# Performance work log

Measured on AMD Instinct MI355X. Metric: run time of the kernel, lower is better.

Reference implementation:

```python
import jax, jax.numpy as jnp
import numpy as np

DIM = 192; H = 6; HD = DIM // H; WS = 8; N = WS * WS; B = 2048; NW = 64
SCALE = HD ** -0.5


def _rel_idx():
    # replicates torch meshgrid (indexing='ij') relative position index
    coords = np.stack(np.meshgrid(np.arange(WS), np.arange(WS), indexing='ij'))  # [2,WS,WS]
    flat = coords.reshape(2, -1)  # [2, N]
    rel = flat[:, :, None] - flat[:, None, :]  # [2, N, N]
    rel = rel.transpose(1, 2, 0).astype(np.int64)
    rel[..., 0] += WS - 1
    rel[..., 1] += WS - 1
    rel[..., 0] *= 2 * WS - 1
    return jnp.asarray(rel.sum(-1), dtype=jnp.int32)  # [N, N]


def setup_inputs() -> dict:
    key = jax.random.key(0)
    ks = jax.random.split(key, 8)
    x1 = jax.random.normal(ks[0], (B, N, DIM), jnp.float32)
    x2 = jax.random.normal(ks[1], (B, N, DIM), jnp.float32)
    mask = jnp.zeros((NW, N, N), jnp.float32)
    qw = jax.random.normal(ks[2], (DIM, DIM), jnp.float32) * 0.02
    qb = jnp.zeros((DIM,), jnp.float32)
    kvw = jax.random.normal(ks[3], (2 * DIM, DIM), jnp.float32) * 0.02
    kvb = jnp.zeros((2 * DIM,), jnp.float32)
    rpb = jax.random.normal(ks[4], ((2 * WS - 1) * (2 * WS - 1), H), jnp.float32) * 0.02
    gamma = jnp.full((1,), 0.5, jnp.float32)  # nonzero to exercise LAM path
    pw = jax.random.normal(ks[5], (DIM, DIM), jnp.float32) * 0.02
    pb = jnp.zeros((DIM,), jnp.float32)
    rel_idx = _rel_idx()
    return {"x1": x1, "x2": x2, "mask": mask, "qw": qw, "qb": qb, "kvw": kvw,
            "kvb": kvb, "rpb": rpb, "gamma": gamma, "pw": pw, "pb": pb,
            "rel_idx": rel_idx}


def reference(x1, x2, mask, qw, qb, kvw, kvb, rpb, gamma, pw, pb, rel_idx):
    # q projection -> [B, H, N, HD], pre-scaled (torch code reassigns q = q*scale)
    q = (x1 @ qw.T + qb).reshape(B, N, H, HD).transpose(0, 2, 1, 3) * SCALE
    kv = (x2 @ kvw.T + kvb).reshape(B, N, 2, H, HD)
    k = kv[:, :, 0].transpose(0, 2, 1, 3)  # [B, H, N, HD]
    v = kv[:, :, 1].transpose(0, 2, 1, 3)
    attn = jnp.einsum('bhnd,bhmd->bhnm', q, k)  # [B, H, N, N]
    # gathered relative position bias [H, N, N]
    bias = rpb[rel_idx.reshape(-1)].reshape(N, N, H).transpose(2, 0, 1)
    attn = attn + bias[None]
    attn = attn.reshape(B // NW, NW, H, N, N) + mask[None, :, None]
    attn = jax.nn.softmax(attn.reshape(B, H, N, N), axis=-1)
    y = jnp.einsum('bhnm,bhmd->bhnd', attn, v)  # [B, H, N, HD]
    # LAM module: channel-wise (dim) attention over (head*num)
    xp = y.transpose(0, 3, 1, 2)              # [B, HD, H, N]
    flat = xp.reshape(B, HD, H * N)
    energy = jnp.einsum('bik,bjk->bij', flat, flat)  # [B, HD, HD]
    # note: original computes energy_new but softmaxes raw energy; replicate
    att = jax.nn.softmax(energy, axis=-1)
    out = jnp.einsum('bij,bjk->bik', att, flat).reshape(B, HD, H, N)
    out = gamma * out + xp
    lam = out.transpose(0, 2, 3, 1)            # [B, H, N, HD]
    x = (lam.transpose(0, 2, 1, 3).reshape(B, N, DIM)
         + q.transpose(0, 2, 1, 3).reshape(B, N, DIM)
         + x1)
    return x @ pw.T + pb
```

## Files before the change

kernel.cpp:

```cpp
#include <hip/hip_runtime.h>

#define DIM 192
#define NTOK 64
#define NHEAD 6
#define HDIM 32
#define SCALE 0.17677669529663687f

typedef __attribute__((ext_vector_type(8))) short bf16x8;
typedef __attribute__((ext_vector_type(4))) float f32x4;

__device__ __forceinline__ ushort f2bf(float f) {
    union { float f; unsigned u; } x; x.f = f;
    unsigned r = x.u + 0x7FFFu + ((x.u >> 16) & 1u);
    return (ushort)(r >> 16);
}
__device__ __forceinline__ float bf2f(ushort h) {
    union { unsigned u; float f; } x; x.u = ((unsigned)h) << 16;
    return x.f;
}

__device__ __forceinline__ f32x4 MF(bf16x8 a, bf16x8 b, f32x4 c) {
    return __builtin_amdgcn_mfma_f32_16x16x32_bf16(a, b, c, 0, 0, 0);
}

__device__ __forceinline__ bf16x8 frag(const ushort* base, int stride, int r0, int k0) {
    const int l = threadIdx.x & 63;
    return *(const bf16x8*)(base + (r0 + (l & 15)) * stride + (k0 + ((l >> 4) << 3)));
}

__global__ void prep_weights(const float* __restrict__ qw, const float* __restrict__ kvw,
                             const float* __restrict__ pw, ushort* __restrict__ wbf) {
    int i = blockIdx.x * 256 + threadIdx.x;
    if (i < 36864) wbf[i] = f2bf(qw[i]);
    else if (i < 110592) wbf[i] = f2bf(kvw[i - 36864]);
    else if (i < 147456) wbf[i] = f2bf(pw[i - 110592]);
}

__global__ void prep_cmb(const float* __restrict__ rpb, const float* __restrict__ mask,
                         ushort* __restrict__ cmb) {
    int t = blockIdx.x * 256 + threadIdx.x;
    int e = t << 2;
    int n0 = e & 63;
    int m  = (e >> 6) & 63;
    int hw = e >> 12;
    int h = hw % 6, w = hw / 6;
#pragma unroll
    for (int j = 0; j < 4; ++j) {
        int n = n0 + j;
        int ridx = ((n >> 3) - (m >> 3) + 7) * 15 + ((n & 7) - (m & 7) + 7);
        float v = rpb[ridx * 6 + h] + mask[(w * 64 + n) * 64 + m];
        cmb[e + j] = f2bf(v);
    }
}

__global__ __launch_bounds__(256, 4) void proj7(
    const float* __restrict__ x1, const float* __restrict__ x2,
    const float* __restrict__ qb, const float* __restrict__ kvb,
    const ushort* __restrict__ qwbf, const ushort* __restrict__ kvwbf,
    ushort* __restrict__ Qf, ushort* __restrict__ Kf, ushort* __restrict__ Vf)
{
    __shared__ __align__(16) ushort sXA[64 * 200];
    __shared__ __align__(16) ushort stg[4 * 1280];
    const int tid = threadIdx.x, wave = tid >> 6, lane = tid & 63;
    const int g = lane >> 4, mcol = lane & 15;
    const int b = blockIdx.x;
    const f32x4 zero4 = {0.f, 0.f, 0.f, 0.f};
    ushort* st = stg + wave * 1280;

    {
        const float4* src = (const float4*)(x2 + (size_t)b * 12288);
        for (int i = tid; i < 3072; i += 256) {
            float4 v = src[i];
            int e = i << 2; int n = e / DIM; int c = e - n * DIM;
            ushort4 w;
            ((ushort*)&w)[0] = f2bf(v.x); ((ushort*)&w)[1] = f2bf(v.y);
            ((ushort*)&w)[2] = f2bf(v.z); ((ushort*)&w)[3] = f2bf(v.w);
            *(ushort4*)(&sXA[n * 200 + c]) = w;
        }
    }
    __syncthreads();

    for (int t = wave; t < 12; t += 4) {
        const int isV = (t >= 6) ? 1 : 0;
        const int h = isV ? (t - 6) : t;
        bf16x8 wf[2][6];
#pragma unroll
        for (int c2 = 0; c2 < 2; ++c2) {
            int ctg = (isV ? (12 + 2 * h) : (2 * h)) + c2;
#pragma unroll
            for (int ks = 0; ks < 6; ++ks)
                wf[c2][ks] = frag(kvwbf, DIM, ctg * 16, ks * 32);
        }
        f32x4 acc[4][2];
#pragma unroll
        for (int rt = 0; rt < 4; ++rt)
#pragma unroll
            for (int c2 = 0; c2 < 2; ++c2) acc[rt][c2] = zero4;
#pragma unroll
        for (int rt = 0; rt < 4; ++rt) {
            bf16x8 af[6];
#pragma unroll
            for (int ks = 0; ks < 6; ++ks) af[ks] = frag(sXA, 200, rt * 16, ks * 32);
#pragma unroll
            for (int c2 = 0; c2 < 2; ++c2)
#pragma unroll
                for (int ks = 0; ks < 6; ++ks)
                    acc[rt][c2] = MF(af[ks], wf[c2][ks], acc[rt][c2]);
        }
        if (!isV) {
#pragma unroll
            for (int ph = 0; ph < 2; ++ph) {
#pragma unroll
                for (int c2 = 0; c2 < 2; ++c2) {
                    float bv = kvb[h * 32 + c2 * 16 + mcol];
#pragma unroll
                    for (int rl = 0; rl < 2; ++rl)
#pragma unroll
                        for (int j = 0; j < 4; ++j)
                            st[(rl * 16 + (g << 2) + j) * 40 + c2 * 16 + mcol] =
                                f2bf(acc[2 * ph + rl][c2][j] + bv);
                }
                asm volatile("s_waitcnt lgkmcnt(0)" ::: "memory");
#pragma unroll
                for (int cl = 0; cl < 2; ++cl) {
                    bf16x8 fr = frag(st, 40, cl * 16, 0);
                    *(bf16x8*)(Kf + ((size_t)(b * 6 + h) * 4 + 2 * ph + cl) * 512 + lane * 8) = fr;
                }
            }
        } else {
#pragma unroll
            for (int c = 0; c < 2; ++c) {
#pragma unroll
                for (int c2 = 0; c2 < 2; ++c2) {
                    float bv = kvb[192 + h * 32 + c2 * 16 + mcol];
#pragma unroll
                    for (int rl = 0; rl < 2; ++rl) {
                        ushort4 w4;
#pragma unroll
                        for (int j = 0; j < 4; ++j)
                            ((ushort*)&w4)[j] = f2bf(acc[2 * c + rl][c2][j] + bv);
                        *(ushort4*)(&st[(c2 * 16 + mcol) * 40 + rl * 16 + (g << 2)]) = w4;
                    }
                }
                asm volatile("s_waitcnt lgkmcnt(0)" ::: "memory");
#pragma unroll
                for (int ctd = 0; ctd < 2; ++ctd) {
                    bf16x8 fr = frag(st, 40, ctd * 16, 0);
                    *(bf16x8*)(Vf + (((size_t)(b * 6 + h) * 2 + c) * 2 + ctd) * 512 + lane * 8) = fr;
                }
            }
        }
    }
    __syncthreads();

    {
        const float4* src = (const float4*)(x1 + (size_t)b * 12288);
        for (int i = tid; i < 3072; i += 256) {
            float4 v = src[i];
            int e = i << 2; int n = e / DIM; int c = e - n * DIM;
            ushort4 w;
            ((ushort*)&w)[0] = f2bf(v.x); ((ushort*)&w)[1] = f2bf(v.y);
            ((ushort*)&w)[2] = f2bf(v.z); ((ushort*)&w)[3] = f2bf(v.w);
            *(ushort4*)(&sXA[n * 200 + c]) = w;
        }
    }
    __syncthreads();

    for (int t = wave; t < 6; t += 4) {
        const int h = t;
        bf16x8 wf[2][6];
#pragma unroll
        for (int c2 = 0; c2 < 2; ++c2)
#pragma unroll
            for (int ks = 0; ks < 6; ++ks)
                wf[c2][ks] = frag(qwbf, DIM, (2 * h + c2) * 16, ks * 32);
        f32x4 acc[4][2];
#pragma unroll
        for (int rt = 0; rt < 4; ++rt)
#pragma unroll
            for (int c2 = 0; c2 < 2; ++c2) acc[rt][c2] = zero4;
#pragma unroll
        for (int rt = 0; rt < 4; ++rt) {
            bf16x8 af[6];
#pragma unroll
            for (int ks = 0; ks < 6; ++ks) af[ks] = frag(sXA, 200, rt * 16, ks * 32);
#pragma unroll
            for (int c2 = 0; c2 < 2; ++c2)
#pragma unroll
                for (int ks = 0; ks < 6; ++ks)
                    acc[rt][c2] = MF(af[ks], wf[c2][ks], acc[rt][c2]);
        }
#pragma unroll
        for (int ph = 0; ph < 2; ++ph) {
#pragma unroll
            for (int c2 = 0; c2 < 2; ++c2) {
                float bv = qb[h * 32 + c2 * 16 + mcol];
#pragma unroll
                for (int rl = 0; rl < 2; ++rl)
#pragma unroll
                    for (int j = 0; j < 4; ++j)
                        st[(rl * 16 + (g << 2) + j) * 40 + c2 * 16 + mcol] =
                            f2bf((acc[2 * ph + rl][c2][j] + bv) * SCALE);
            }
            asm volatile("s_waitcnt lgkmcnt(0)" ::: "memory");
#pragma unroll
            for (int cl = 0; cl < 2; ++cl) {
                bf16x8 fr = frag(st, 40, cl * 16, 0);
                *(bf16x8*)(Qf + ((size_t)(b * 6 + h) * 4 + 2 * ph + cl) * 512 + lane * 8) = fr;
            }
        }
    }
}

__global__ __launch_bounds__(256, 4) void attn_heads(
    const ushort* __restrict__ Qf, ushort* KfY,
    const ushort* __restrict__ Vf, const ushort* __restrict__ cmb)
{
    __shared__ __align__(16) ushort sP[4 * 1280];
    const int tid = threadIdx.x, wave = tid >> 6, lane = tid & 63;
    const int g = lane >> 4, mcol = lane & 15;
    const int gid = blockIdx.x * 4 + wave;
    const int w = gid / 6, h = gid - 6 * (gid / 6);
    const f32x4 zero4 = {0.f, 0.f, 0.f, 0.f};

    const ushort* qp = Qf  + (size_t)gid * 2048;
    ushort*       kp = KfY + (size_t)gid * 2048;
    const ushort* vp = Vf  + (size_t)gid * 2048;
    const ushort* cp = cmb + (size_t)((w & 63) * 6 + h) * 4096;
    ushort* slot = sP + wave * 1280;

    bf16x8 kb[4], vb[4];
#pragma unroll
    for (int ct = 0; ct < 4; ++ct) kb[ct] = *(const bf16x8*)(kp + ct * 512 + lane * 8);
#pragma unroll
    for (int c = 0; c < 4; ++c) vb[c] = *(const bf16x8*)(vp + c * 512 + lane * 8);

    ushort4 y4[4][2];
#pragma unroll
    for (int rt = 0; rt < 4; ++rt) {
        bf16x8 qa = *(const bf16x8*)(qp + rt * 512 + lane * 8);
        f32x4 acc[4];
#pragma unroll
        for (int ct = 0; ct < 4; ++ct) acc[ct] = MF(qa, kb[ct], zero4);
#pragma unroll
        for (int ct = 0; ct < 4; ++ct) {
            ushort4 b4 = *(const ushort4*)(cp + (ct * 16 + mcol) * 64 + rt * 16 + (g << 2));
#pragma unroll
            for (int j = 0; j < 4; ++j) acc[ct][j] += bf2f(((ushort*)&b4)[j]);
        }
        float sm[4];
#pragma unroll
        for (int j = 0; j < 4; ++j) {
            float v = fmaxf(fmaxf(acc[0][j], acc[1][j]), fmaxf(acc[2][j], acc[3][j]));
            v = fmaxf(v, __shfl_xor(v, 1, 64));
            v = fmaxf(v, __shfl_xor(v, 2, 64));
            v = fmaxf(v, __shfl_xor(v, 4, 64));
            v = fmaxf(v, __shfl_xor(v, 8, 64));
            float s = 0.f;
#pragma unroll
            for (int ct = 0; ct < 4; ++ct) {
                float p = __expf(acc[ct][j] - v);
                acc[ct][j] = p; s += p;
            }
            s += __shfl_xor(s, 1, 64);
            s += __shfl_xor(s, 2, 64);
            s += __shfl_xor(s, 4, 64);
            s += __shfl_xor(s, 8, 64);
            sm[j] = 1.0f / s;
        }
#pragma unroll
        for (int ct = 0; ct < 4; ++ct)
#pragma unroll
            for (int j = 0; j < 4; ++j)
                slot[((g << 2) + j) * 72 + ct * 16 + mcol] = f2bf(acc[ct][j] * sm[j]);
        asm volatile("s_waitcnt lgkmcnt(0)" ::: "memory");
        f32x4 ay0 = zero4, ay1 = zero4;
#pragma unroll
        for (int c = 0; c < 2; ++c) {
            bf16x8 pa = frag(slot, 72, 0, c * 32);
            ay0 = MF(pa, vb[c * 2 + 0], ay0);
            ay1 = MF(pa, vb[c * 2 + 1], ay1);
        }
#pragma unroll
        for (int j = 0; j < 4; ++j) {
            ((ushort*)&y4[rt][0])[j] = f2bf(ay0[j]);
            ((ushort*)&y4[rt][1])[j] = f2bf(ay1[j]);
        }
    }
#pragma unroll
    for (int rt = 0; rt < 4; ++rt)
#pragma unroll
        for (int ctd = 0; ctd < 2; ++ctd)
            *(ushort4*)(kp + (ctd * 16 + mcol) * 64 + rt * 16 + (g << 2)) = y4[rt][ctd];
}

__global__ __launch_bounds__(256, 4) void lam_proj(
    const ushort* __restrict__ Yd, const ushort* __restrict__ Qf,
    const float* __restrict__ x1, const float* __restrict__ gammap,
    const ushort* __restrict__ pwbf, const float* __restrict__ pb,
    float* __restrict__ out)
{
    __shared__ __align__(16) ushort sYF[13824];
    __shared__ __align__(16) float  sE[32 * 33];
    __shared__ __align__(16) ushort sAtt[32 * 40];

    const int tid = threadIdx.x, wave = tid >> 6, lane = tid & 63;
    const int g = lane >> 4, mcol = lane & 15;
    const int b = blockIdx.x;
    const float gamma = gammap[0];
    const f32x4 zero4 = {0.f, 0.f, 0.f, 0.f};

    {
        const ushort* src = Yd + (size_t)b * 12288;
        for (int i = tid; i < 1536; i += 256) {
            int hd = i >> 8;
            int rem = i & 255;
            int row = rem >> 3, k8 = rem & 7;
            uint4 v = *(const uint4*)(src + hd * 2048 + row * 64 + k8 * 8);
            *(uint4*)(&sYF[hd * 2304 + row * 72 + k8 * 8]) = v;
        }
    }
    __syncthreads();

    {
        int rt = wave >> 1, ct = wave & 1;
        f32x4 a0 = zero4, a1 = zero4;
#pragma unroll
        for (int hd = 0; hd < 6; hd += 2) {
            const ushort* Y0 = sYF + hd * 2304;
            const ushort* Y1 = sYF + (hd + 1) * 2304;
#pragma unroll
            for (int kk = 0; kk < 2; ++kk) {
                a0 = MF(frag(Y0, 72, rt * 16, kk * 32), frag(Y0, 72, ct * 16, kk * 32), a0);
                a1 = MF(frag(Y1, 72, rt * 16, kk * 32), frag(Y1, 72, ct * 16, kk * 32), a1);
            }
        }
        f32x4 acc = a0 + a1;
#pragma unroll
        for (int j = 0; j < 4; ++j)
            sE[(rt * 16 + (g << 2) + j) * 33 + ct * 16 + mcol] = acc[j];
    }
    __syncthreads();

    {
        int r = tid >> 3, l8 = tid & 7;
        float e[4];
        float mx = -1e30f;
#pragma unroll
        for (int k = 0; k < 4; ++k) { e[k] = sE[r * 33 + l8 + k * 8]; mx = fmaxf(mx, e[k]); }
        mx = fmaxf(mx, __shfl_xor(mx, 1, 64));
        mx = fmaxf(mx, __shfl_xor(mx, 2, 64));
        mx = fmaxf(mx, __shfl_xor(mx, 4, 64));
        float s = 0.f;
#pragma unroll
        for (int k = 0; k < 4; ++k) { e[k] = __expf(e[k] - mx); s += e[k]; }
        s += __shfl_xor(s, 1, 64);
        s += __shfl_xor(s, 2, 64);
        s += __shfl_xor(s, 4, 64);
        float rs = 1.0f / s;
#pragma unroll
        for (int k = 0; k < 4; ++k) sAtt[r * 40 + l8 + k * 8] = f2bf(e[k] * rs);
    }
    __syncthreads();

    bf16x8 aa01[2];
    aa01[0] = frag(sAtt, 40, 0, 0);
    aa01[1] = frag(sAtt, 40, 16, 0);
    ushort4 w4st[12];
#pragma unroll
    for (int i = 0; i < 12; ++i) {
        int t = wave + i * 4;
        int rtL = t & 1, ct = t >> 1;
        int col = ct * 16 + mcol;
        int hh = col >> 6, nn = col & 63;
        const ushort* Yh = sYF + hh * 2304;
        bf16x8 bb;
#pragma unroll
        for (int jj = 0; jj < 8; ++jj) bb[jj] = (short)Yh[((g << 3) + jj) * 72 + nn];
        f32x4 acc = MF(aa01[rtL], bb, zero4);
        int d0 = rtL * 16 + (g << 2);
        ushort4 qv4 = *(const ushort4*)(Qf + (size_t)(b * 6 + hh) * 2048 +
                                        (nn >> 4) * 512 + ((nn & 15) + ((d0 >> 3) << 4)) * 8 + (d0 & 7));
        float4 xv4 = *(const float4*)(x1 + (size_t)b * 12288 + nn * 192 + hh * 32 + d0);
        ushort4 w4;
#pragma unroll
        for (int j = 0; j < 4; ++j) {
            float flatv = bf2f(Yh[(d0 + j) * 72 + nn]);
            float val = gamma * acc[j] + flatv + bf2f(((ushort*)&qv4)[j]) + ((const float*)&xv4)[j];
            ((ushort*)&w4)[j] = f2bf(val);
        }
        w4st[i] = w4;
    }
    __syncthreads();
#pragma unroll
    for (int i = 0; i < 12; ++i) {
        int t = wave + i * 4;
        int rtL = t & 1, ct = t >> 1;
        int col = ct * 16 + mcol;
        int hh = col >> 6, nn = col & 63;
        int d0 = rtL * 16 + (g << 2);
        *(ushort4*)(&sYF[nn * 200 + hh * 32 + d0]) = w4st[i];
    }
    __syncthreads();

    {
        float* outp = out + (size_t)b * 12288;
        const int rt = wave;
        bf16x8 af[6];
#pragma unroll
        for (int ks = 0; ks < 6; ++ks) af[ks] = frag(sYF, 200, rt * 16, ks * 32);
#pragma unroll 2
        for (int ct = 0; ct < 12; ++ct) {
            f32x4 acc = zero4;
#pragma unroll
            for (int ks = 0; ks < 6; ++ks)
                acc = MF(af[ks], frag(pwbf, DIM, ct * 16, ks * 32), acc);
            int co = ct * 16 + mcol;
            float pbv = pb[co];
#pragma unroll
            for (int j = 0; j < 4; ++j)
                outp[(rt * 16 + (g << 2) + j) * DIM + co] = acc[j] + pbv;
        }
    }
}

extern "C" void kernel_launch(void* const* d_in, const int* in_sizes, int n_in,
                              void* d_out, int out_size, void* d_ws, size_t ws_size,
                              hipStream_t stream) {
    const float* x1    = (const float*)d_in[0];
    const float* x2    = (const float*)d_in[1];
    const float* mask  = (const float*)d_in[2];
    const float* qw    = (const float*)d_in[3];
    const float* qbv   = (const float*)d_in[4];
    const float* kvw   = (const float*)d_in[5];
    const float* kvbv  = (const float*)d_in[6];
    const float* rpb   = (const float*)d_in[7];
    const float* gamma = (const float*)d_in[8];
    const float* pw    = (const float*)d_in[9];
    const float* pbv   = (const float*)d_in[10];
    ushort* wbf = (ushort*)d_ws;

    prep_weights<<<576, 256, 0, stream>>>(qw, kvw, pw, wbf);

    ushort* cmb = wbf + 147456;
    ushort* Qf  = wbf + 1720320;
    ushort* Kf  = wbf + 26886144;
    ushort* Vf  = wbf + 52051968;
    prep_cmb<<<1536, 256, 0, stream>>>(rpb, mask, cmb);
    proj7<<<2048, 256, 0, stream>>>(x1, x2, qbv, kvbv,
                                    wbf, wbf + 36864, Qf, Kf, Vf);
    attn_heads<<<3072, 256, 0, stream>>>(Qf, Kf, Vf, cmb);
    lam_proj<<<2048, 256, 0, stream>>>(Kf, Qf, x1, gamma,
                                       wbf + 110592, pbv, (float*)d_out);
}
```

Before: 269.7 us.

## Split projection into separate Q and KV blocks and precompute Q+x1 residual

The projection kernel now launches two blocks per batch element, one handling the K/V projection from x2 and one handling the Q projection from x1, instead of doing both sequentially in one block. This gives more parallelism and a shorter critical path per block. When the workspace is large enough, the Q block also writes a bf16 residual buffer holding q plus the bf16-rounded x1, so lam_proj reads one bf16 value instead of Q plus fp32 x1. The cost is an extra global write of the residual buffer and a larger grid, with slight extra rounding because x1 is added in bf16.

```diff
diff --git a/kernel.cpp b/kernel.cpp
--- a/kernel.cpp
+++ b/kernel.cpp
@@ -53,22 +53,24 @@
     }
 }
 
-__global__ __launch_bounds__(256, 4) void proj7(
+__global__ __launch_bounds__(256, 4) void proj7s(
     const float* __restrict__ x1, const float* __restrict__ x2,
     const float* __restrict__ qb, const float* __restrict__ kvb,
     const ushort* __restrict__ qwbf, const ushort* __restrict__ kvwbf,
-    ushort* __restrict__ Qf, ushort* __restrict__ Kf, ushort* __restrict__ Vf)
+    ushort* __restrict__ Qf, ushort* __restrict__ Kf, ushort* __restrict__ Vf,
+    ushort* __restrict__ Rf, int hasRf)
 {
     __shared__ __align__(16) ushort sXA[64 * 200];
     __shared__ __align__(16) ushort stg[4 * 1280];
     const int tid = threadIdx.x, wave = tid >> 6, lane = tid & 63;
     const int g = lane >> 4, mcol = lane & 15;
-    const int b = blockIdx.x;
+    const int b = blockIdx.x >> 1;
+    const int isQ = blockIdx.x & 1;
     const f32x4 zero4 = {0.f, 0.f, 0.f, 0.f};
     ushort* st = stg + wave * 1280;
 
     {
-        const float4* src = (const float4*)(x2 + (size_t)b * 12288);
+        const float4* src = (const float4*)((isQ ? x1 : x2) + (size_t)b * 12288);
         for (int i = tid; i < 3072; i += 256) {
             float4 v = src[i];
             int e = i << 2; int n = e / DIM; int c = e - n * DIM;
@@ -80,133 +82,143 @@
     }
     __syncthreads();
 
-    for (int t = wave; t < 12; t += 4) {
-        const int isV = (t >= 6) ? 1 : 0;
-        const int h = isV ? (t - 6) : t;
-        bf16x8 wf[2][6];
-#pragma unroll
-        for (int c2 = 0; c2 < 2; ++c2) {
-            int ctg = (isV ? (12 + 2 * h) : (2 * h)) + c2;
-#pragma unroll
-            for (int ks = 0; ks < 6; ++ks)
-                wf[c2][ks] = frag(kvwbf, DIM, ctg * 16, ks * 32);
-        }
-        f32x4 acc[4][2];
-#pragma unroll
-        for (int rt = 0; rt < 4; ++rt)
-#pragma unroll
-            for (int c2 = 0; c2 < 2; ++c2) acc[rt][c2] = zero4;
-#pragma unroll
-        for (int rt = 0; rt < 4; ++rt) {
-            bf16x8 af[6];
-#pragma unroll
-            for (int ks = 0; ks < 6; ++ks) af[ks] = frag(sXA, 200, rt * 16, ks * 32);
+    if (!isQ) {
+        for (int t = wave; t < 12; t += 4) {
+            const int isV = (t >= 6) ? 1 : 0;
+            const int h = isV ? (t - 6) : t;
+            bf16x8 wf[2][6];
+#pragma unroll
+            for (int c2 = 0; c2 < 2; ++c2) {
+                int ctg = (isV ? (12 + 2 * h) : (2 * h)) + c2;
+#pragma unroll
+                for (int ks = 0; ks < 6; ++ks)
+                    wf[c2][ks] = frag(kvwbf, DIM, ctg * 16, ks * 32);
+            }
+            f32x4 acc[4][2];
+#pragma unroll
+            for (int rt = 0; rt < 4; ++rt)
+#pragma unroll
+                for (int c2 = 0; c2 < 2; ++c2) acc[rt][c2] = zero4;
+#pragma unroll
+            for (int rt = 0; rt < 4; ++rt) {
+                bf16x8 af[6];
+#pragma unroll
+                for (int ks = 0; ks < 6; ++ks) af[ks] = frag(sXA, 200, rt * 16, ks * 32);
+#pragma unroll
+                for (int c2 = 0; c2 < 2; ++c2)
+#pragma unroll
+                    for (int ks = 0; ks < 6; ++ks)
+                        acc[rt][c2] = MF(af[ks], wf[c2][ks], acc[rt][c2]);
+            }
+            if (!isV) {
+#pragma unroll
+                for (int ph = 0; ph < 2; ++ph) {
+#pragma unroll
+                    for (int c2 = 0; c2 < 2; ++c2) {
+                        float bv = kvb[h * 32 + c2 * 16 + mcol];
+#pragma unroll
+                        for (int rl = 0; rl < 2; ++rl)
+#pragma unroll
+                            for (int j = 0; j < 4; ++j)
+                                st[(rl * 16 + (g << 2) + j) * 40 + c2 * 16 + mcol] =
+                                    f2bf(acc[2 * ph + rl][c2][j] + bv);
+                    }
+                    asm volatile("s_waitcnt lgkmcnt(0)" ::: "memory");
+#pragma unroll
+                    for (int cl = 0; cl < 2; ++cl) {
+                        bf16x8 fr = frag(st, 40, cl * 16, 0);
+                        *(bf16x8*)(Kf + ((size_t)(b * 6 + h) * 4 + 2 * ph + cl) * 512 + lane * 8) = fr;
+                    }
+                }
+            } else {
+#pragma unroll
+                for (int c = 0; c < 2; ++c) {
+#pragma unroll
+                    for (int c2 = 0; c2 < 2; ++c2) {
+                        float bv = kvb[192 + h * 32 + c2 * 16 + mcol];
+#pragma unroll
+                        for (int rl = 0; rl < 2; ++rl) {
+                            ushort4 w4;
+#pragma unroll
+                            for (int j = 0; j < 4; ++j)
+                                ((ushort*)&w4)[j] = f2bf(acc[2 * c + rl][c2][j] + bv);
+                            *(ushort4*)(&st[(c2 * 16 + mcol) * 40 + rl * 16 + (g << 2)]) = w4;
+                        }
+                    }
+                    asm volatile("s_waitcnt lgkmcnt(0)" ::: "memory");
+#pragma unroll
+                    for (int ctd = 0; ctd < 2; ++ctd) {
+                        bf16x8 fr = frag(st, 40, ctd * 16, 0);
+                        *(bf16x8*)(Vf + (((size_t)(b * 6 + h) * 2 + c) * 2 + ctd) * 512 + lane * 8) = fr;
+                    }
+                }
+            }
+        }
+    } else {
+        for (int t = wave; t < 6; t += 4) {
+            const int h = t;
+            bf16x8 wf[2][6];
 #pragma unroll
             for (int c2 = 0; c2 < 2; ++c2)
 #pragma unroll
                 for (int ks = 0; ks < 6; ++ks)
-                    acc[rt][c2] = MF(af[ks], wf[c2][ks], acc[rt][c2]);
-        }
-        if (!isV) {
+                    wf[c2][ks] = frag(qwbf, DIM, (2 * h + c2) * 16, ks * 32);
+            f32x4 acc[4][2];
+#pragma unroll
+            for (int rt = 0; rt < 4; ++rt)
+#pragma unroll
+                for (int c2 = 0; c2 < 2; ++c2) acc[rt][c2] = zero4;
+#pragma unroll
+            for (int rt = 0; rt < 4; ++rt) {
+                bf16x8 af[6];
+#pragma unroll
+                for (int ks = 0; ks < 6; ++ks) af[ks] = frag(sXA, 200, rt * 16, ks * 32);
+#pragma unroll
+                for (int c2 = 0; c2 < 2; ++c2)
+#pragma unroll
+                    for (int ks = 0; ks < 6; ++ks)
+                        acc[rt][c2] = MF(af[ks], wf[c2][ks], acc[rt][c2]);
+            }
 #pragma unroll
             for (int ph = 0; ph < 2; ++ph) {
 #pragma unroll
                 for (int c2 = 0; c2 < 2; ++c2) {
-                    float bv = kvb[h * 32 + c2 * 16 + mcol];
+                    float bv = qb[h * 32 + c2 * 16 + mcol];
 #pragma unroll
                     for (int rl = 0; rl < 2; ++rl)
 #pragma unroll
                         for (int j = 0; j < 4; ++j)
                             st[(rl * 16 + (g << 2) + j) * 40 + c2 * 16 + mcol] =
-                                f2bf(acc[2 * ph + rl][c2][j] + bv);
+                                f2bf((acc[2 * ph + rl][c2][j] + bv) * SCALE);
                 }
                 asm volatile("s_waitcnt lgkmcnt(0)" ::: "memory");
 #pragma unroll
                 for (int cl = 0; cl < 2; ++cl) {
                     bf16x8 fr = frag(st, 40, cl * 16, 0);
-                    *(bf16x8*)(Kf + ((size_t)(b * 6 + h) * 4 + 2 * ph + cl) * 512 + lane * 8) = fr;
+                    *(bf16x8*)(Qf + ((size_t)(b * 6 + h) * 4 + 2 * ph + cl) * 512 + lane * 8) = fr;
                 }
-            }
-        } else {
-#pragma unroll
-            for (int c = 0; c < 2; ++c) {
-#pragma unroll
-                for (int c2 = 0; c2 < 2; ++c2) {
-                    float bv = kvb[192 + h * 32 + c2 * 16 + mcol];
-#pragma unroll
-                    for (int rl = 0; rl < 2; ++rl) {
-                        ushort4 w4;
-#pragma unroll
-                        for (int j = 0; j < 4; ++j)
-                            ((ushort*)&w4)[j] = f2bf(acc[2 * c + rl][c2][j] + bv);
-                        *(ushort4*)(&st[(c2 * 16 + mcol) * 40 + rl * 16 + (g << 2)]) = w4;
+                if (hasRf) {
+#pragma unroll
+                    for (int c2 = 0; c2 < 2; ++c2) {
+                        float bv = qb[h * 32 + c2 * 16 + mcol];
+#pragma unroll
+                        for (int rl = 0; rl < 2; ++rl)
+#pragma unroll
+                            for (int j = 0; j < 4; ++j) {
+                                int row = 2 * ph + rl;
+                                float qv = (acc[row][c2][j] + bv) * SCALE;
+                                float xv = bf2f(sXA[(ph * 32 + rl * 16 + (g << 2) + j) * 200 +
+                                                    h * 32 + c2 * 16 + mcol]);
+                                st[(rl * 16 + (g << 2) + j) * 40 + c2 * 16 + mcol] = f2bf(qv + xv);
+                            }
+                    }
+                    asm volatile("s_waitcnt lgkmcnt(0)" ::: "memory");
+#pragma unroll
+                    for (int cl = 0; cl < 2; ++cl) {
+                        bf16x8 fr = frag(st, 40, cl * 16, 0);
+                        *(bf16x8*)(Rf + ((size_t)(b * 6 + h) * 4 + 2 * ph + cl) * 512 + lane * 8) = fr;
                     }
                 }
-                asm volatile("s_waitcnt lgkmcnt(0)" ::: "memory");
-#pragma unroll
-                for (int ctd = 0; ctd < 2; ++ctd) {
-                    bf16x8 fr = frag(st, 40, ctd * 16, 0);
-                    *(bf16x8*)(Vf + (((size_t)(b * 6 + h) * 2 + c) * 2 + ctd) * 512 + lane * 8) = fr;
-                }
-            }
-        }
-    }
-    __syncthreads();
-
-    {
-        const float4* src = (const float4*)(x1 + (size_t)b * 12288);
-        for (int i = tid; i < 3072; i += 256) {
-            float4 v = src[i];
-            int e = i << 2; int n = e / DIM; int c = e - n * DIM;
-            ushort4 w;
-            ((ushort*)&w)[0] = f2bf(v.x); ((ushort*)&w)[1] = f2bf(v.y);
-            ((ushort*)&w)[2] = f2bf(v.z); ((ushort*)&w)[3] = f2bf(v.w);
-            *(ushort4*)(&sXA[n * 200 + c]) = w;
-        }
-    }
-    __syncthreads();
-
-    for (int t = wave; t < 6; t += 4) {
-        const int h = t;
-        bf16x8 wf[2][6];
-#pragma unroll
-        for (int c2 = 0; c2 < 2; ++c2)
-#pragma unroll
-            for (int ks = 0; ks < 6; ++ks)
-                wf[c2][ks] = frag(qwbf, DIM, (2 * h + c2) * 16, ks * 32);
-        f32x4 acc[4][2];
-#pragma unroll
-        for (int rt = 0; rt < 4; ++rt)
-#pragma unroll
-            for (int c2 = 0; c2 < 2; ++c2) acc[rt][c2] = zero4;
-#pragma unroll
-        for (int rt = 0; rt < 4; ++rt) {
-            bf16x8 af[6];
-#pragma unroll
-            for (int ks = 0; ks < 6; ++ks) af[ks] = frag(sXA, 200, rt * 16, ks * 32);
-#pragma unroll
-            for (int c2 = 0; c2 < 2; ++c2)
-#pragma unroll
-                for (int ks = 0; ks < 6; ++ks)
-                    acc[rt][c2] = MF(af[ks], wf[c2][ks], acc[rt][c2]);
-        }
-#pragma unroll
-        for (int ph = 0; ph < 2; ++ph) {
-#pragma unroll
-            for (int c2 = 0; c2 < 2; ++c2) {
-                float bv = qb[h * 32 + c2 * 16 + mcol];
-#pragma unroll
-                for (int rl = 0; rl < 2; ++rl)
-#pragma unroll
-                    for (int j = 0; j < 4; ++j)
-                        st[(rl * 16 + (g << 2) + j) * 40 + c2 * 16 + mcol] =
-                            f2bf((acc[2 * ph + rl][c2][j] + bv) * SCALE);
-            }
-            asm volatile("s_waitcnt lgkmcnt(0)" ::: "memory");
-#pragma unroll
-            for (int cl = 0; cl < 2; ++cl) {
-                bf16x8 fr = frag(st, 40, cl * 16, 0);
-                *(bf16x8*)(Qf + ((size_t)(b * 6 + h) * 4 + 2 * ph + cl) * 512 + lane * 8) = fr;
             }
         }
     }
@@ -298,7 +310,7 @@
     const ushort* __restrict__ Yd, const ushort* __restrict__ Qf,
     const float* __restrict__ x1, const float* __restrict__ gammap,
     const ushort* __restrict__ pwbf, const float* __restrict__ pb,
-    float* __restrict__ out)
+    float* __restrict__ out, const ushort* __restrict__ Rf, int useRf)
 {
     __shared__ __align__(16) ushort sYF[13824];
     __shared__ __align__(16) float  sE[32 * 33];
@@ -379,15 +391,26 @@
         for (int jj = 0; jj < 8; ++jj) bb[jj] = (short)Yh[((g << 3) + jj) * 72 + nn];
         f32x4 acc = MF(aa01[rtL], bb, zero4);
         int d0 = rtL * 16 + (g << 2);
-        ushort4 qv4 = *(const ushort4*)(Qf + (size_t)(b * 6 + hh) * 2048 +
-                                        (nn >> 4) * 512 + ((nn & 15) + ((d0 >> 3) << 4)) * 8 + (d0 & 7));
-        float4 xv4 = *(const float4*)(x1 + (size_t)b * 12288 + nn * 192 + hh * 32 + d0);
         ushort4 w4;
-#pragma unroll
-        for (int j = 0; j < 4; ++j) {
-            float flatv = bf2f(Yh[(d0 + j) * 72 + nn]);
-            float val = gamma * acc[j] + flatv + bf2f(((ushort*)&qv4)[j]) + ((const float*)&xv4)[j];
-            ((ushort*)&w4)[j] = f2bf(val);
+        if (useRf) {
+            ushort4 rv4 = *(const ushort4*)(Rf + (size_t)(b * 6 + hh) * 2048 +
+                                            (nn >> 4) * 512 + ((nn & 15) + ((d0 >> 3) << 4)) * 8 + (d0 & 7));
+#pragma unroll
+            for (int j = 0; j < 4; ++j) {
+                float flatv = bf2f(Yh[(d0 + j) * 72 + nn]);
+                float val = gamma * acc[j] + flatv + bf2f(((ushort*)&rv4)[j]);
+                ((ushort*)&w4)[j] = f2bf(val);
+            }
+        } else {
+            ushort4 qv4 = *(const ushort4*)(Qf + (size_t)(b * 6 + hh) * 2048 +
+                                            (nn >> 4) * 512 + ((nn & 15) + ((d0 >> 3) << 4)) * 8 + (d0 & 7));
+            float4 xv4 = *(const float4*)(x1 + (size_t)b * 12288 + nn * 192 + hh * 32 + d0);
+#pragma unroll
+            for (int j = 0; j < 4; ++j) {
+                float flatv = bf2f(Yh[(d0 + j) * 72 + nn]);
+                float val = gamma * acc[j] + flatv + bf2f(((ushort*)&qv4)[j]) + ((const float*)&xv4)[j];
+                ((ushort*)&w4)[j] = f2bf(val);
+            }
         }
         w4st[i] = w4;
     }
@@ -446,10 +469,13 @@
     ushort* Qf  = wbf + 1720320;
     ushort* Kf  = wbf + 26886144;
     ushort* Vf  = wbf + 52051968;
+    ushort* Rf  = wbf + 77217792;
+    const int useRf = (ws_size >= 204767232u) ? 1 : 0;
+
     prep_cmb<<<1536, 256, 0, stream>>>(rpb, mask, cmb);
-    proj7<<<2048, 256, 0, stream>>>(x1, x2, qbv, kvbv,
-                                    wbf, wbf + 36864, Qf, Kf, Vf);
+    proj7s<<<4096, 256, 0, stream>>>(x1, x2, qbv, kvbv,
+                                     wbf, wbf + 36864, Qf, Kf, Vf, Rf, useRf);
     attn_heads<<<3072, 256, 0, stream>>>(Qf, Kf, Vf, cmb);
     lam_proj<<<2048, 256, 0, stream>>>(Kf, Qf, x1, gamma,
-                                       wbf + 110592, pbv, (float*)d_out);
-}
+                                       wbf + 110592, pbv, (float*)d_out, Rf, useRf);
+}
```

Result: slower. 286.0 us (+6.0%).

## Fuse QKV projection and per-head window attention into one kernel

Applied to the files above, without the earlier changes.

Merges the projection kernel and the attention kernel into a single 384-thread block, one wave per head. K, V and Q fragments stay in registers and are consumed directly by the attention softmax and PV product, so the K and V global round trip and one kernel launch disappear. The block now stages both x1 and x2 in shared memory and uses 6 waves, which raises LDS and register use per block and lowers the number of resident blocks. Q is still written to global memory for the later LAM stage.

```diff
diff --git a/kernel.cpp b/kernel.cpp
--- a/kernel.cpp
+++ b/kernel.cpp
@@ -53,14 +53,16 @@
     }
 }
 
-__global__ __launch_bounds__(256, 4) void proj7(
+__global__ __launch_bounds__(384, 2) void proj_attn(
     const float* __restrict__ x1, const float* __restrict__ x2,
     const float* __restrict__ qb, const float* __restrict__ kvb,
     const ushort* __restrict__ qwbf, const ushort* __restrict__ kvwbf,
-    ushort* __restrict__ Qf, ushort* __restrict__ Kf, ushort* __restrict__ Vf)
+    const ushort* __restrict__ cmb,
+    ushort* __restrict__ Qf, ushort* __restrict__ KfY)
 {
-    __shared__ __align__(16) ushort sXA[64 * 200];
-    __shared__ __align__(16) ushort stg[4 * 1280];
+    __shared__ __align__(16) ushort sX1[64 * 200];
+    __shared__ __align__(16) ushort sX2[64 * 200];
+    __shared__ __align__(16) ushort stg[6 * 1280];
     const int tid = threadIdx.x, wave = tid >> 6, lane = tid & 63;
     const int g = lane >> 4, mcol = lane & 15;
     const int b = blockIdx.x;
@@ -68,106 +70,119 @@
     ushort* st = stg + wave * 1280;
 
     {
-        const float4* src = (const float4*)(x2 + (size_t)b * 12288);
-        for (int i = tid; i < 3072; i += 256) {
-            float4 v = src[i];
+        const float4* s1 = (const float4*)(x1 + (size_t)b * 12288);
+        const float4* s2 = (const float4*)(x2 + (size_t)b * 12288);
+        for (int i = tid; i < 3072; i += 384) {
+            float4 v = s1[i];
             int e = i << 2; int n = e / DIM; int c = e - n * DIM;
             ushort4 w;
             ((ushort*)&w)[0] = f2bf(v.x); ((ushort*)&w)[1] = f2bf(v.y);
             ((ushort*)&w)[2] = f2bf(v.z); ((ushort*)&w)[3] = f2bf(v.w);
-            *(ushort4*)(&sXA[n * 200 + c]) = w;
-        }
-    }
-    __syncthreads();
-
-    for (int t = wave; t < 12; t += 4) {
-        const int isV = (t >= 6) ? 1 : 0;
-        const int h = isV ? (t - 6) : t;
-        bf16x8 wf[2][6];
-#pragma unroll
-        for (int c2 = 0; c2 < 2; ++c2) {
-            int ctg = (isV ? (12 + 2 * h) : (2 * h)) + c2;
-#pragma unroll
-            for (int ks = 0; ks < 6; ++ks)
-                wf[c2][ks] = frag(kvwbf, DIM, ctg * 16, ks * 32);
-        }
-        f32x4 acc[4][2];
-#pragma unroll
-        for (int rt = 0; rt < 4; ++rt)
-#pragma unroll
-            for (int c2 = 0; c2 < 2; ++c2) acc[rt][c2] = zero4;
-#pragma unroll
-        for (int rt = 0; rt < 4; ++rt) {
-            bf16x8 af[6];
-#pragma unroll
-            for (int ks = 0; ks < 6; ++ks) af[ks] = frag(sXA, 200, rt * 16, ks * 32);
-#pragma unroll
-            for (int c2 = 0; c2 < 2; ++c2)
-#pragma unroll
-                for (int ks = 0; ks < 6; ++ks)
-                    acc[rt][c2] = MF(af[ks], wf[c2][ks], acc[rt][c2]);
-        }
-        if (!isV) {
-#pragma unroll
-            for (int ph = 0; ph < 2; ++ph) {
-#pragma unroll
-                for (int c2 = 0; c2 < 2; ++c2) {
-                    float bv = kvb[h * 32 + c2 * 16 + mcol];
-#pragma unroll
-                    for (int rl = 0; rl < 2; ++rl)
-#pragma unroll
-                        for (int j = 0; j < 4; ++j)
-                            st[(rl * 16 + (g << 2) + j) * 40 + c2 * 16 + mcol] =
-                                f2bf(acc[2 * ph + rl][c2][j] + bv);
-                }
-                asm volatile("s_waitcnt lgkmcnt(0)" ::: "memory");
-#pragma unroll
-                for (int cl = 0; cl < 2; ++cl) {
-                    bf16x8 fr = frag(st, 40, cl * 16, 0);
-                    *(bf16x8*)(Kf + ((size_t)(b * 6 + h) * 4 + 2 * ph + cl) * 512 + lane * 8) = fr;
-                }
-            }
-        } else {
-#pragma unroll
-            for (int c = 0; c < 2; ++c) {
-#pragma unroll
-                for (int c2 = 0; c2 < 2; ++c2) {
-                    float bv = kvb[192 + h * 32 + c2 * 16 + mcol];
-#pragma unroll
-                    for (int rl = 0; rl < 2; ++rl) {
-                        ushort4 w4;
-#pragma unroll
-                        for (int j = 0; j < 4; ++j)
-                            ((ushort*)&w4)[j] = f2bf(acc[2 * c + rl][c2][j] + bv);
-                        *(ushort4*)(&st[(c2 * 16 + mcol) * 40 + rl * 16 + (g << 2)]) = w4;
-                    }
-                }
-                asm volatile("s_waitcnt lgkmcnt(0)" ::: "memory");
-#pragma unroll
-                for (int ctd = 0; ctd < 2; ++ctd) {
-                    bf16x8 fr = frag(st, 40, ctd * 16, 0);
-                    *(bf16x8*)(Vf + (((size_t)(b * 6 + h) * 2 + c) * 2 + ctd) * 512 + lane * 8) = fr;
-                }
-            }
-        }
-    }
-    __syncthreads();
-
-    {
-        const float4* src = (const float4*)(x1 + (size_t)b * 12288);
-        for (int i = tid; i < 3072; i += 256) {
-            float4 v = src[i];
+            *(ushort4*)(&sX1[n * 200 + c]) = w;
+        }
+        for (int i = tid; i < 3072; i += 384) {
+            float4 v = s2[i];
             int e = i << 2; int n = e / DIM; int c = e - n * DIM;
             ushort4 w;
             ((ushort*)&w)[0] = f2bf(v.x); ((ushort*)&w)[1] = f2bf(v.y);
             ((ushort*)&w)[2] = f2bf(v.z); ((ushort*)&w)[3] = f2bf(v.w);
-            *(ushort4*)(&sXA[n * 200 + c]) = w;
-        }
-    }
-    __syncthreads();
-
-    for (int t = wave; t < 6; t += 4) {
-        const int h = t;
+            *(ushort4*)(&sX2[n * 200 + c]) = w;
+        }
+    }
+    __syncthreads();
+
+    const int h = wave;
+    bf16x8 kb[4], vb[4], qa[4];
+
+    {
+        bf16x8 wf[2][6];
+#pragma unroll
+        for (int c2 = 0; c2 < 2; ++c2)
+#pragma unroll
+            for (int ks = 0; ks < 6; ++ks)
+                wf[c2][ks] = frag(kvwbf, DIM, (2 * h + c2) * 16, ks * 32);
+        f32x4 acc[4][2];
+#pragma unroll
+        for (int rt = 0; rt < 4; ++rt)
+#pragma unroll
+            for (int c2 = 0; c2 < 2; ++c2) acc[rt][c2] = zero4;
+#pragma unroll
+        for (int rt = 0; rt < 4; ++rt) {
+            bf16x8 af[6];
+#pragma unroll
+            for (int ks = 0; ks < 6; ++ks) af[ks] = frag(sX2, 200, rt * 16, ks * 32);
+#pragma unroll
+            for (int c2 = 0; c2 < 2; ++c2)
+#pragma unroll
+                for (int ks = 0; ks < 6; ++ks)
+                    acc[rt][c2] = MF(af[ks], wf[c2][ks], acc[rt][c2]);
+        }
+#pragma unroll
+        for (int ph = 0; ph < 2; ++ph) {
+#pragma unroll
+            for (int c2 = 0; c2 < 2; ++c2) {
+                float bv = kvb[h * 32 + c2 * 16 + mcol];
+#pragma unroll
+                for (int rl = 0; rl < 2; ++rl)
+#pragma unroll
+                    for (int j = 0; j < 4; ++j)
+                        st[(rl * 16 + (g << 2) + j) * 40 + c2 * 16 + mcol] =
+                            f2bf(acc[2 * ph + rl][c2][j] + bv);
+            }
+            asm volatile("s_waitcnt lgkmcnt(0)" ::: "memory");
+#pragma unroll
+            for (int cl = 0; cl < 2; ++cl)
+                kb[2 * ph + cl] = frag(st, 40, cl * 16, 0);
+            asm volatile("s_waitcnt lgkmcnt(0)" ::: "memory");
+        }
+    }
+
+    {
+        bf16x8 wf[2][6];
+#pragma unroll
+        for (int c2 = 0; c2 < 2; ++c2)
+#pragma unroll
+            for (int ks = 0; ks < 6; ++ks)
+                wf[c2][ks] = frag(kvwbf, DIM, (12 + 2 * h + c2) * 16, ks * 32);
+        f32x4 acc[4][2];
+#pragma unroll
+        for (int rt = 0; rt < 4; ++rt)
+#pragma unroll
+            for (int c2 = 0; c2 < 2; ++c2) acc[rt][c2] = zero4;
+#pragma unroll
+        for (int rt = 0; rt < 4; ++rt) {
+            bf16x8 af[6];
+#pragma unroll
+            for (int ks = 0; ks < 6; ++ks) af[ks] = frag(sX2, 200, rt * 16, ks * 32);
+#pragma unroll
+            for (int c2 = 0; c2 < 2; ++c2)
+#pragma unroll
+                for (int ks = 0; ks < 6; ++ks)
+                    acc[rt][c2] = MF(af[ks], wf[c2][ks], acc[rt][c2]);
+        }
+#pragma unroll
+        for (int c = 0; c < 2; ++c) {
+#pragma unroll
+            for (int c2 = 0; c2 < 2; ++c2) {
+                float bv = kvb[192 + h * 32 + c2 * 16 + mcol];
+#pragma unroll
+                for (int rl = 0; rl < 2; ++rl) {
+                    ushort4 w4;
+#pragma unroll
+                    for (int j = 0; j < 4; ++j)
+                        ((ushort*)&w4)[j] = f2bf(acc[2 * c + rl][c2][j] + bv);
+                    *(ushort4*)(&st[(c2 * 16 + mcol) * 40 + rl * 16 + (g << 2)]) = w4;
+                }
+            }
+            asm volatile("s_waitcnt lgkmcnt(0)" ::: "memory");
+#pragma unroll
+            for (int ctd = 0; ctd < 2; ++ctd)
+                vb[c * 2 + ctd] = frag(st, 40, ctd * 16, 0);
+            asm volatile("s_waitcnt lgkmcnt(0)" ::: "memory");
+        }
+    }
+
+    {
         bf16x8 wf[2][6];
 #pragma unroll
         for (int c2 = 0; c2 < 2; ++c2)
@@ -183,7 +198,7 @@
         for (int rt = 0; rt < 4; ++rt) {
             bf16x8 af[6];
 #pragma unroll
-            for (int ks = 0; ks < 6; ++ks) af[ks] = frag(sXA, 200, rt * 16, ks * 32);
+            for (int ks = 0; ks < 6; ++ks) af[ks] = frag(sX1, 200, rt * 16, ks * 32);
 #pragma unroll
             for (int c2 = 0; c2 < 2; ++c2)
 #pragma unroll
@@ -205,93 +220,75 @@
             asm volatile("s_waitcnt lgkmcnt(0)" ::: "memory");
 #pragma unroll
             for (int cl = 0; cl < 2; ++cl) {
-                bf16x8 fr = frag(st, 40, cl * 16, 0);
-                *(bf16x8*)(Qf + ((size_t)(b * 6 + h) * 4 + 2 * ph + cl) * 512 + lane * 8) = fr;
-            }
-        }
-    }
-}
-
-__global__ __launch_bounds__(256, 4) void attn_heads(
-    const ushort* __restrict__ Qf, ushort* KfY,
-    const ushort* __restrict__ Vf, const ushort* __restrict__ cmb)
-{
-    __shared__ __align__(16) ushort sP[4 * 1280];
-    const int tid = threadIdx.x, wave = tid >> 6, lane = tid & 63;
-    const int g = lane >> 4, mcol = lane & 15;
-    const int gid = blockIdx.x * 4 + wave;
-    const int w = gid / 6, h = gid - 6 * (gid / 6);
-    const f32x4 zero4 = {0.f, 0.f, 0.f, 0.f};
-
-    const ushort* qp = Qf  + (size_t)gid * 2048;
-    ushort*       kp = KfY + (size_t)gid * 2048;
-    const ushort* vp = Vf  + (size_t)gid * 2048;
-    const ushort* cp = cmb + (size_t)((w & 63) * 6 + h) * 4096;
-    ushort* slot = sP + wave * 1280;
-
-    bf16x8 kb[4], vb[4];
-#pragma unroll
-    for (int ct = 0; ct < 4; ++ct) kb[ct] = *(const bf16x8*)(kp + ct * 512 + lane * 8);
-#pragma unroll
-    for (int c = 0; c < 4; ++c) vb[c] = *(const bf16x8*)(vp + c * 512 + lane * 8);
-
-    ushort4 y4[4][2];
-#pragma unroll
-    for (int rt = 0; rt < 4; ++rt) {
-        bf16x8 qa = *(const bf16x8*)(qp + rt * 512 + lane * 8);
-        f32x4 acc[4];
-#pragma unroll
-        for (int ct = 0; ct < 4; ++ct) acc[ct] = MF(qa, kb[ct], zero4);
-#pragma unroll
-        for (int ct = 0; ct < 4; ++ct) {
-            ushort4 b4 = *(const ushort4*)(cp + (ct * 16 + mcol) * 64 + rt * 16 + (g << 2));
-#pragma unroll
-            for (int j = 0; j < 4; ++j) acc[ct][j] += bf2f(((ushort*)&b4)[j]);
-        }
-        float sm[4];
-#pragma unroll
-        for (int j = 0; j < 4; ++j) {
-            float v = fmaxf(fmaxf(acc[0][j], acc[1][j]), fmaxf(acc[2][j], acc[3][j]));
-            v = fmaxf(v, __shfl_xor(v, 1, 64));
-            v = fmaxf(v, __shfl_xor(v, 2, 64));
-            v = fmaxf(v, __shfl_xor(v, 4, 64));
-            v = fmaxf(v, __shfl_xor(v, 8, 64));
-            float s = 0.f;
+                qa[2 * ph + cl] = frag(st, 40, cl * 16, 0);
+                *(bf16x8*)(Qf + ((size_t)(b * 6 + h) * 4 + 2 * ph + cl) * 512 + lane * 8) =
+                    qa[2 * ph + cl];
+            }
+            asm volatile("s_waitcnt lgkmcnt(0)" ::: "memory");
+        }
+    }
+
+    {
+        const ushort* cp = cmb + (size_t)((b & 63) * 6 + h) * 4096;
+        ushort* kpY = KfY + (size_t)(b * 6 + h) * 2048;
+        ushort4 y4[4][2];
+#pragma unroll
+        for (int rt = 0; rt < 4; ++rt) {
+            f32x4 acc[4];
+#pragma unroll
+            for (int ct = 0; ct < 4; ++ct) acc[ct] = MF(qa[rt], kb[ct], zero4);
 #pragma unroll
             for (int ct = 0; ct < 4; ++ct) {
-                float p = __expf(acc[ct][j] - v);
-                acc[ct][j] = p; s += p;
-            }
-            s += __shfl_xor(s, 1, 64);
-            s += __shfl_xor(s, 2, 64);
-            s += __shfl_xor(s, 4, 64);
-            s += __shfl_xor(s, 8, 64);
-            sm[j] = 1.0f / s;
-        }
-#pragma unroll
-        for (int ct = 0; ct < 4; ++ct)
-#pragma unroll
-            for (int j = 0; j < 4; ++j)
-                slot[((g << 2) + j) * 72 + ct * 16 + mcol] = f2bf(acc[ct][j] * sm[j]);
-        asm volatile("s_waitcnt lgkmcnt(0)" ::: "memory");
-        f32x4 ay0 = zero4, ay1 = zero4;
-#pragma unroll
-        for (int c = 0; c < 2; ++c) {
-            bf16x8 pa = frag(slot, 72, 0, c * 32);
-            ay0 = MF(pa, vb[c * 2 + 0], ay0);
-            ay1 = MF(pa, vb[c * 2 + 1], ay1);
-        }
-#pragma unroll
-        for (int j = 0; j < 4; ++j) {
-            ((ushort*)&y4[rt][0])[j] = f2bf(ay0[j]);
-            ((ushort*)&y4[rt][1])[j] = f2bf(ay1[j]);
-        }
-    }
-#pragma unroll
-    for (int rt = 0; rt < 4; ++rt)
-#pragma unroll
-        for (int ctd = 0; ctd < 2; ++ctd)
-            *(ushort4*)(kp + (ctd * 16 + mcol) * 64 + rt * 16 + (g << 2)) = y4[rt][ctd];
+                ushort4 b4 = *(const ushort4*)(cp + (ct * 16 + mcol) * 64 + rt * 16 + (g << 2));
+#pragma unroll
+                for (int j = 0; j < 4; ++j) acc[ct][j] += bf2f(((ushort*)&b4)[j]);
+            }
+            float sm[4];
+#pragma unroll
+            for (int j = 0; j < 4; ++j) {
+                float v = fmaxf(fmaxf(acc[0][j], acc[1][j]), fmaxf(acc[2][j], acc[3][j]));
+                v = fmaxf(v, __shfl_xor(v, 1, 64));
+                v = fmaxf(v, __shfl_xor(v, 2, 64));
+                v = fmaxf(v, __shfl_xor(v, 4, 64));
+                v = fmaxf(v, __shfl_xor(v, 8, 64));
+                float s = 0.f;
+#pragma unroll
+                for (int ct = 0; ct < 4; ++ct) {
+                    float p = __expf(acc[ct][j] - v);
+                    acc[ct][j] = p; s += p;
+                }
+                s += __shfl_xor(s, 1, 64);
+                s += __shfl_xor(s, 2, 64);
+                s += __shfl_xor(s, 4, 64);
+                s += __shfl_xor(s, 8, 64);
+                sm[j] = 1.0f / s;
+            }
+#pragma unroll
+            for (int ct = 0; ct < 4; ++ct)
+#pragma unroll
+                for (int j = 0; j < 4; ++j)
+                    st[((g << 2) + j) * 72 + ct * 16 + mcol] = f2bf(acc[ct][j] * sm[j]);
+            asm volatile("s_waitcnt lgkmcnt(0)" ::: "memory");
+            f32x4 ay0 = zero4, ay1 = zero4;
+#pragma unroll
+            for (int c = 0; c < 2; ++c) {
+                bf16x8 pa = frag(st, 72, 0, c * 32);
+                ay0 = MF(pa, vb[c * 2 + 0], ay0);
+                ay1 = MF(pa, vb[c * 2 + 1], ay1);
+            }
+            asm volatile("s_waitcnt lgkmcnt(0)" ::: "memory");
+#pragma unroll
+            for (int j = 0; j < 4; ++j) {
+                ((ushort*)&y4[rt][0])[j] = f2bf(ay0[j]);
+                ((ushort*)&y4[rt][1])[j] = f2bf(ay1[j]);
+            }
+        }
+#pragma unroll
+        for (int rt = 0; rt < 4; ++rt)
+#pragma unroll
+            for (int ctd = 0; ctd < 2; ++ctd)
+                *(ushort4*)(kpY + (ctd * 16 + mcol) * 64 + rt * 16 + (g << 2)) = y4[rt][ctd];
+    }
 }
 
 __global__ __launch_bounds__(256, 4) void lam_proj(
@@ -444,12 +441,10 @@
 
     ushort* cmb = wbf + 147456;
     ushort* Qf  = wbf + 1720320;
-    ushort* Kf  = wbf + 26886144;
-    ushort* Vf  = wbf + 52051968;
+    ushort* KfY = wbf + 26886144;
     prep_cmb<<<1536, 256, 0, stream>>>(rpb, mask, cmb);
-    proj7<<<2048, 256, 0, stream>>>(x1, x2, qbv, kvbv,
-                                    wbf, wbf + 36864, Qf, Kf, Vf);
-    attn_heads<<<3072, 256, 0, stream>>>(Qf, Kf, Vf, cmb);
-    lam_proj<<<2048, 256, 0, stream>>>(Kf, Qf, x1, gamma,
+    proj_attn<<<2048, 384, 0, stream>>>(x1, x2, qbv, kvbv,
+                                        wbf, wbf + 36864, cmb, Qf, KfY);
+    lam_proj<<<2048, 256, 0, stream>>>(KfY, Qf, x1, gamma,
                                        wbf + 110592, pbv, (float*)d_out);
 }
```

Measured after the change: 311.7 us. 1.16x slower.
